# Performance work log

Measured on AMD Instinct MI355X. Metric: run time of the kernel, lower is better.

Reference implementation:

```python
import jax, jax.numpy as jnp
import numpy as np

N = 16384
NFEAT = 128
NCLASS = 2


def setup_inputs() -> dict:
    key = jax.random.key(0)
    ks = jax.random.split(key, 12)
    x = jax.random.normal(ks[0], (N, NFEAT), dtype=jnp.float32)
    # dense (normalized-ish) adjacency, scaled so aggregated features stay O(1)
    adj = jax.random.uniform(ks[1], (N, N), dtype=jnp.float32) * (2.0 / N)
    idx_map = jax.random.randint(ks[2], (N,), 0, N)
    s = lambda f: 1.0 / np.sqrt(f)
    W1 = jax.random.normal(ks[3], (NFEAT, 32), dtype=jnp.float32) * s(NFEAT)
    b1 = jax.random.normal(ks[4], (32,), dtype=jnp.float32) * 0.01
    W2 = jax.random.normal(ks[5], (32, 48), dtype=jnp.float32) * s(32)
    b2 = jax.random.normal(ks[6], (48,), dtype=jnp.float32) * 0.01
    W3 = jax.random.normal(ks[7], (48, 64), dtype=jnp.float32) * s(48)
    b3 = jax.random.normal(ks[8], (64,), dtype=jnp.float32) * 0.01
    fcW1 = jax.random.normal(ks[9], (64, 32), dtype=jnp.float32) * s(64)
    fcb1 = jnp.zeros((32,), dtype=jnp.float32)
    fcW2 = jax.random.normal(ks[10], (32, NCLASS), dtype=jnp.float32) * s(32)
    fcb2 = jnp.zeros((NCLASS,), dtype=jnp.float32)
    return {"x": x, "adj": adj, "idx_map": idx_map,
            "W1": W1, "b1": b1, "W2": W2, "b2": b2, "W3": W3, "b3": b3,
            "fcW1": fcW1, "fcb1": fcb1, "fcW2": fcW2, "fcb2": fcb2}


def _gc(x, adj, W, b):
    # GraphConvolution (Kipf): adj @ (x @ W) + b
    return adj @ (x @ W) + b


def reference(x, adj, idx_map, W1, b1, W2, b2, W3, b3, fcW1, fcb1, fcW2, fcb2):
    # eval mode: dropout is identity
    h = jax.nn.relu(_gc(x, adj, W1, b1))   # [N, 32]
    h = jax.nn.relu(_gc(h, adj, W2, b2))   # [N, 48]
    h = jax.nn.relu(_gc(h, adj, W3, b3))   # [N, 64]
    y = jnp.mean(h, axis=0)                # [64] graph readout
    y = jax.nn.relu(y @ fcW1 + fcb1)       # [32]
    y = jax.nn.softmax(y @ fcW2 + fcb2, axis=0)  # [NCLASS]
    return y
```

## Files before the change

### kernel.cpp

```cpp
#include <hip/hip_runtime.h>
#include <hip/hip_bf16.h>

typedef float  f32x4  __attribute__((ext_vector_type(4)));
typedef __bf16 bf16x8 __attribute__((ext_vector_type(8)));
typedef unsigned short u16x8 __attribute__((ext_vector_type(8)));

#define NN 16384

__device__ inline bf16x8 cvt_bf16x8(f32x4 a, f32x4 b) {
    bf16x8 r;
    r[0] = (__bf16)a[0]; r[1] = (__bf16)a[1]; r[2] = (__bf16)a[2]; r[3] = (__bf16)a[3];
    r[4] = (__bf16)b[0]; r[5] = (__bf16)b[1]; r[6] = (__bf16)b[2]; r[7] = (__bf16)b[3];
    return r;
}

template<int FIN, int FOUT>
__global__ __launch_bounds__(256) void xw_t_kernel(
    const float* __restrict__ H, const float* __restrict__ W,
    unsigned short* __restrict__ Tt)
{
    __shared__ float sh[64][FIN + 1];
    const int n0 = blockIdx.x * 64;
    for (int i = threadIdx.x; i < 64 * FIN; i += 256) {
        sh[i / FIN][i % FIN] = H[(size_t)n0 * FIN + i];
    }
    __syncthreads();
    const int nl = threadIdx.x & 63;
    const int f0 = threadIdx.x >> 6;
    for (int f = f0; f < FOUT; f += 4) {
        float s = 0.f;
        #pragma unroll 8
        for (int k = 0; k < FIN; ++k) s += sh[nl][k] * W[k * FOUT + f];
        __bf16 h = (__bf16)s;
        Tt[(size_t)f * NN + n0 + nl] = __builtin_bit_cast(unsigned short, h);
    }
}

template<int NCB>
__global__ __launch_bounds__(256) void gc_kernel(
    const float* __restrict__ adj, const unsigned short* __restrict__ Tt,
    const float* __restrict__ bias, float* __restrict__ H)
{
    constexpr int F = NCB * 16;
    const int lane = threadIdx.x & 63;
    const int wave = threadIdx.x >> 6;
    const int rb   = blockIdx.x * 4 + wave;
    const int m    = lane & 15;
    const int kq   = lane >> 4;

    const float* ap = adj + (size_t)(rb * 16 + m) * NN + kq * 8;
    const unsigned short* bp[NCB];
    f32x4 acc[NCB];
    #pragma unroll
    for (int cb = 0; cb < NCB; ++cb) {
        bp[cb] = Tt + (size_t)(cb * 16 + m) * NN + kq * 8;
        acc[cb] = (f32x4){0.f, 0.f, 0.f, 0.f};
    }

    #pragma unroll 4
    for (int kb = 0; kb < NN / 32; ++kb) {
        const f32x4* a4 = (const f32x4*)(ap + kb * 32);
        f32x4 a0 = a4[0];
        f32x4 a1 = a4[1];
        bf16x8 af = cvt_bf16x8(a0, a1);
        #pragma unroll
        for (int cb = 0; cb < NCB; ++cb) {
            bf16x8 bf = __builtin_bit_cast(bf16x8, *(const u16x8*)(bp[cb] + kb * 32));
            acc[cb] = __builtin_amdgcn_mfma_f32_16x16x32_bf16(af, bf, acc[cb], 0, 0, 0);
        }
    }

    #pragma unroll
    for (int cb = 0; cb < NCB; ++cb) {
        const int c = cb * 16 + m;
        const float bv = bias[c];
        #pragma unroll
        for (int i = 0; i < 4; ++i) {
            const int r = rb * 16 + kq * 4 + i;
            H[(size_t)r * F + c] = fmaxf(acc[cb][i] + bv, 0.f);
        }
    }
}

__global__ __launch_bounds__(256) void reduce_cols_kernel(
    const float* __restrict__ H3, float* __restrict__ P)
{
    __shared__ float sm[256];
    const int t = threadIdx.x;
    const int c = t & 63;
    const int rg = t >> 6;
    const int r0 = blockIdx.x * 256;
    float s = 0.f;
    #pragma unroll 4
    for (int j = 0; j < 64; ++j) {
        const int r = r0 + rg + j * 4;
        s += H3[(size_t)r * 64 + c];
    }
    sm[t] = s;
    __syncthreads();
    if (t < 64) P[blockIdx.x * 64 + t] = sm[t] + sm[t + 64] + sm[t + 128] + sm[t + 192];
}

__global__ void head_kernel(
    const float* __restrict__ P,
    const float* __restrict__ fcW1, const float* __restrict__ fcb1,
    const float* __restrict__ fcW2, const float* __restrict__ fcb2,
    float* __restrict__ out)
{
    __shared__ float y[64];
    __shared__ float z1[32];
    __shared__ float lg[2];
    const int t = threadIdx.x;
    float s = 0.f;
    for (int w = 0; w < 64; ++w) s += P[w * 64 + t];
    y[t] = s * (1.0f / 16384.0f);
    __syncthreads();
    if (t < 32) {
        float a = fcb1[t];
        for (int k = 0; k < 64; ++k) a += y[k] * fcW1[k * 32 + t];
        z1[t] = fmaxf(a, 0.f);
    }
    __syncthreads();
    if (t < 2) {
        float a = fcb2[t];
        for (int j = 0; j < 32; ++j) a += z1[j] * fcW2[j * 2 + t];
        lg[t] = a;
    }
    __syncthreads();
    if (t == 0) {
        const float mx = fmaxf(lg[0], lg[1]);
        const float e0 = expf(lg[0] - mx), e1 = expf(lg[1] - mx);
        out[0] = e0 / (e0 + e1);
        out[1] = e1 / (e0 + e1);
    }
}

extern "C" void kernel_launch(void* const* d_in, const int* in_sizes, int n_in,
                              void* d_out, int out_size, void* d_ws, size_t ws_size,
                              hipStream_t stream) {
    const float* x     = (const float*)d_in[0];
    const float* adj   = (const float*)d_in[1];
    const float* W1    = (const float*)d_in[3];
    const float* b1    = (const float*)d_in[4];
    const float* W2    = (const float*)d_in[5];
    const float* b2    = (const float*)d_in[6];
    const float* W3    = (const float*)d_in[7];
    const float* b3    = (const float*)d_in[8];
    const float* fcW1  = (const float*)d_in[9];
    const float* fcb1  = (const float*)d_in[10];
    const float* fcW2  = (const float*)d_in[11];
    const float* fcb2  = (const float*)d_in[12];
    float* out = (float*)d_out;

    char* ws = (char*)d_ws;
    unsigned short* Tt = (unsigned short*)(ws + 0);
    float* H1 = (float*)(ws + (2u << 20));
    float* H2 = (float*)(ws + (4u << 20));
    float* H3 = (float*)(ws + (8u << 20));
    float* P  = (float*)(ws + (12u << 20));

    xw_t_kernel<128, 32><<<NN / 64, 256, 0, stream>>>(x, W1, Tt);
    gc_kernel<2><<<256, 256, 0, stream>>>(adj, Tt, b1, H1);
    xw_t_kernel<32, 48><<<NN / 64, 256, 0, stream>>>(H1, W2, Tt);
    gc_kernel<3><<<256, 256, 0, stream>>>(adj, Tt, b2, H2);
    xw_t_kernel<48, 64><<<NN / 64, 256, 0, stream>>>(H2, W3, Tt);
    gc_kernel<4><<<256, 256, 0, stream>>>(adj, Tt, b3, H3);
    reduce_cols_kernel<<<64, 256, 0, stream>>>(H3, P);
    head_kernel<<<1, 64, 0, stream>>>(P, fcW1, fcb1, fcW2, fcb2, out);
}
```

Before: 2.140 ms.

## Cache bf16 copy of adjacency and split K across waves for more parallelism

The first graph-conv kernel converts the fp32 adjacency to bf16 and writes it to workspace, and the later two layers read that half-size copy. Each block now covers 16 rows with its four waves splitting the K dimension and reducing partial sums through shared memory. The grid grows fourfold, which raises occupancy. This adds a 512 MiB workspace write and a shared-memory reduction.

Result: no change. 2.171 ms (+1.5%).

```diff
diff --git a/kernel.cpp b/kernel.cpp
--- a/kernel.cpp
+++ b/kernel.cpp
@@ -37,32 +37,38 @@
 }
 
 template<int NCB>
-__global__ __launch_bounds__(256) void gc_kernel(
-    const float* __restrict__ adj, const unsigned short* __restrict__ Tt,
+__global__ __launch_bounds__(256) void gc1_kernel(
+    const float* __restrict__ adj, unsigned short* __restrict__ adjb,
+    const unsigned short* __restrict__ Tt,
     const float* __restrict__ bias, float* __restrict__ H)
 {
     constexpr int F = NCB * 16;
+    constexpr int KC = NN / 4;
     const int lane = threadIdx.x & 63;
     const int wave = threadIdx.x >> 6;
-    const int rb   = blockIdx.x * 4 + wave;
+    const int rb   = blockIdx.x;
     const int m    = lane & 15;
     const int kq   = lane >> 4;
-
-    const float* ap = adj + (size_t)(rb * 16 + m) * NN + kq * 8;
+    const int k0   = wave * KC;
+
+    const size_t row = (size_t)(rb * 16 + m);
+    const float* ap = adj + row * NN + k0 + kq * 8;
+    unsigned short* wp = adjb + row * NN + k0 + kq * 8;
     const unsigned short* bp[NCB];
     f32x4 acc[NCB];
     #pragma unroll
     for (int cb = 0; cb < NCB; ++cb) {
-        bp[cb] = Tt + (size_t)(cb * 16 + m) * NN + kq * 8;
+        bp[cb] = Tt + (size_t)(cb * 16 + m) * NN + k0 + kq * 8;
         acc[cb] = (f32x4){0.f, 0.f, 0.f, 0.f};
     }
 
     #pragma unroll 4
-    for (int kb = 0; kb < NN / 32; ++kb) {
+    for (int kb = 0; kb < KC / 32; ++kb) {
         const f32x4* a4 = (const f32x4*)(ap + kb * 32);
         f32x4 a0 = a4[0];
         f32x4 a1 = a4[1];
         bf16x8 af = cvt_bf16x8(a0, a1);
+        *(u16x8*)(wp + kb * 32) = __builtin_bit_cast(u16x8, af);
         #pragma unroll
         for (int cb = 0; cb < NCB; ++cb) {
             bf16x8 bf = __builtin_bit_cast(bf16x8, *(const u16x8*)(bp[cb] + kb * 32));
@@ -70,14 +76,83 @@
         }
     }
 
+    __shared__ float red[4][64][NCB * 4];
+    #pragma unroll
+    for (int cb = 0; cb < NCB; ++cb)
+        #pragma unroll
+        for (int i = 0; i < 4; ++i)
+            red[wave][lane][cb * 4 + i] = acc[cb][i];
+    __syncthreads();
+    if (wave == 0) {
+        #pragma unroll
+        for (int cb = 0; cb < NCB; ++cb) {
+            const int c = cb * 16 + m;
+            const float bv = bias[c];
+            #pragma unroll
+            for (int i = 0; i < 4; ++i) {
+                const float s = red[0][lane][cb * 4 + i] + red[1][lane][cb * 4 + i]
+                              + red[2][lane][cb * 4 + i] + red[3][lane][cb * 4 + i];
+                const int r = rb * 16 + kq * 4 + i;
+                H[(size_t)r * F + c] = fmaxf(s + bv + bias[c] * 0.f, 0.f);
+            }
+        }
+    }
+}
+
+template<int NCB>
+__global__ __launch_bounds__(256) void gcb_kernel(
+    const unsigned short* __restrict__ adjb,
+    const unsigned short* __restrict__ Tt,
+    const float* __restrict__ bias, float* __restrict__ H)
+{
+    constexpr int F = NCB * 16;
+    constexpr int KC = NN / 4;
+    const int lane = threadIdx.x & 63;
+    const int wave = threadIdx.x >> 6;
+    const int rb   = blockIdx.x;
+    const int m    = lane & 15;
+    const int kq   = lane >> 4;
+    const int k0   = wave * KC;
+
+    const size_t row = (size_t)(rb * 16 + m);
+    const unsigned short* ap = adjb + row * NN + k0 + kq * 8;
+    const unsigned short* bp[NCB];
+    f32x4 acc[NCB];
     #pragma unroll
     for (int cb = 0; cb < NCB; ++cb) {
-        const int c = cb * 16 + m;
-        const float bv = bias[c];
-        #pragma unroll
-        for (int i = 0; i < 4; ++i) {
-            const int r = rb * 16 + kq * 4 + i;
-            H[(size_t)r * F + c] = fmaxf(acc[cb][i] + bv, 0.f);
+        bp[cb] = Tt + (size_t)(cb * 16 + m) * NN + k0 + kq * 8;
+        acc[cb] = (f32x4){0.f, 0.f, 0.f, 0.f};
+    }
+
+    #pragma unroll 4
+    for (int kb = 0; kb < KC / 32; ++kb) {
+        bf16x8 af = __builtin_bit_cast(bf16x8, *(const u16x8*)(ap + kb * 32));
+        #pragma unroll
+        for (int cb = 0; cb < NCB; ++cb) {
+            bf16x8 bf = __builtin_bit_cast(bf16x8, *(const u16x8*)(bp[cb] + kb * 32));
+            acc[cb] = __builtin_amdgcn_mfma_f32_16x16x32_bf16(af, bf, acc[cb], 0, 0, 0);
+        }
+    }
+
+    __shared__ float red[4][64][NCB * 4];
+    #pragma unroll
+    for (int cb = 0; cb < NCB; ++cb)
+        #pragma unroll
+        for (int i = 0; i < 4; ++i)
+            red[wave][lane][cb * 4 + i] = acc[cb][i];
+    __syncthreads();
+    if (wave == 0) {
+        #pragma unroll
+        for (int cb = 0; cb < NCB; ++cb) {
+            const int c = cb * 16 + m;
+            const float bv = bias[c];
+            #pragma unroll
+            for (int i = 0; i < 4; ++i) {
+                const float s = red[0][lane][cb * 4 + i] + red[1][lane][cb * 4 + i]
+                              + red[2][lane][cb * 4 + i] + red[3][lane][cb * 4 + i];
+                const int r = rb * 16 + kq * 4 + i;
+                H[(size_t)r * F + c] = fmaxf(s + bv, 0.f);
+            }
         }
     }
 }
@@ -87,14 +162,13 @@
 {
     __shared__ float sm[256];
     const int t = threadIdx.x;
-    const int c = t & 63;
     const int rg = t >> 6;
     const int r0 = blockIdx.x * 256;
     float s = 0.f;
     #pragma unroll 4
     for (int j = 0; j < 64; ++j) {
         const int r = r0 + rg + j * 4;
-        s += H3[(size_t)r * 64 + c];
+        s += H3[(size_t)r * 64 + (t & 63)];
     }
     sm[t] = s;
     __syncthreads();
@@ -153,18 +227,20 @@
     float* out = (float*)d_out;
 
     char* ws = (char*)d_ws;
-    unsigned short* Tt = (unsigned short*)(ws + 0);
-    float* H1 = (float*)(ws + (2u << 20));
-    float* H2 = (float*)(ws + (4u << 20));
-    float* H3 = (float*)(ws + (8u << 20));
-    float* P  = (float*)(ws + (12u << 20));
+    unsigned short* adjb = (unsigned short*)(ws + 0);
+    size_t off = (size_t)NN * NN * sizeof(unsigned short);
+    unsigned short* Tt = (unsigned short*)(ws + off);
+    float* H1 = (float*)(ws + off + (2u << 20));
+    float* H2 = (float*)(ws + off + (6u << 20));
+    float* H3 = (float*)(ws + off + (10u << 20));
+    float* P  = (float*)(ws + off + (15u << 20));
 
     xw_t_kernel<128, 32><<<NN / 64, 256, 0, stream>>>(x, W1, Tt);
-    gc_kernel<2><<<256, 256, 0, stream>>>(adj, Tt, b1, H1);
+    gc1_kernel<2><<<NN / 16, 256, 0, stream>>>(adj, adjb, Tt, b1, H1);
     xw_t_kernel<32, 48><<<NN / 64, 256, 0, stream>>>(H1, W2, Tt);
-    gc_kernel<3><<<256, 256, 0, stream>>>(adj, Tt, b2, H2);
+    gcb_kernel<3><<<NN / 16, 256, 0, stream>>>(adjb, Tt, b2, H2);
     xw_t_kernel<48, 64><<<NN / 64, 256, 0, stream>>>(H2, W3, Tt);
-    gc_kernel<4><<<256, 256, 0, stream>>>(adj, Tt, b3, H3);
+    gcb_kernel<4><<<NN / 16, 256, 0, stream>>>(adjb, Tt, b3, H3);
     reduce_cols_kernel<<<64, 256, 0, stream>>>(H3, P);
     head_kernel<<<1, 64, 0, stream>>>(P, fcW1, fcb1, fcW2, fcb2, out);
 }
```
